# Optimization experiments

Measured on AMD Instinct MI355X. Metric: run time of the kernel, lower is better.

## Reference

```python
import jax, jax.numpy as jnp
import numpy as np

E = 8          # num_experts
D = 512        # embed_dim
FF = 4         # ff_mult
H = D * FF     # hidden
B, N = 4, 2048
TOP_K = 2


def setup_inputs() -> dict:
    key = jax.random.key(0)
    ks = jax.random.split(key, 6)
    tokens = jax.random.normal(ks[0], (B, N, D), dtype=jnp.float32)
    # token-choice top-k routing: logits -> top-2 experts per token
    logits = jax.random.normal(ks[1], (B, N, E), dtype=jnp.float32)
    topv, topi = jax.lax.top_k(logits, TOP_K)            # (B,N,K)
    disp = jnp.zeros((B, N, E), jnp.float32)
    disp = jnp.take_along_axis(disp, topi, axis=-1)  # placeholder shape trick avoided below
    disp = jnp.zeros((B, N, E), jnp.float32).at[
        jnp.arange(B)[:, None, None], jnp.arange(N)[None, :, None], topi
    ].set(1.0)                                            # (B,N,E) 0/1 dispatch mask
    w = jax.nn.softmax(topv, axis=-1)                     # combine weights over selected
    comb = jnp.zeros((B, N, E), jnp.float32).at[
        jnp.arange(B)[:, None, None], jnp.arange(N)[None, :, None], topi
    ].set(w)
    # expert params (xavier-ish scale); out_proj gain 0.02 as in module init
    Wg = jax.random.normal(ks[2], (E, D, H), dtype=jnp.float32) * (2.0 / (D + H)) ** 0.5
    Wv = jax.random.normal(ks[3], (E, D, H), dtype=jnp.float32) * (2.0 / (D + H)) ** 0.5
    Wo = jax.random.normal(ks[4], (E, H, D), dtype=jnp.float32) * 0.02 * (2.0 / (D + H)) ** 0.5
    scales = jnp.full((E,), 1.0 / E, dtype=jnp.float32)   # output_scale per expert
    return {"tokens": tokens, "dispatch_weights": disp, "combine_weights": comb,
            "Wg": Wg, "Wv": Wv, "Wo": Wo, "scales": scales}


def reference(tokens, dispatch_weights, combine_weights, Wg, Wv, Wo, scales):
    """ExpertPool.forward: per-expert SwiGLU FFN, combined by routing weights.

    Dense-masked formulation (same math as gather->FFN->weighted scatter-add:
    expert outputs only contribute where dispatch>0).
    """
    b, n, d = tokens.shape
    x = tokens.reshape(b * n, d)                          # (M, D)
    gate = jax.nn.gelu(jnp.einsum('md,edh->emh', x, Wg), approximate=False)
    value = jnp.einsum('md,edh->emh', x, Wv)
    out_e = jnp.einsum('emh,ehd->emd', gate * value, Wo) * scales[:, None, None]
    mask = dispatch_weights.reshape(b * n, -1) > 0        # (M, E)
    w = jnp.where(mask, combine_weights.reshape(b * n, -1), 0.0)
    out = jnp.einsum('emd,me->md', out_e, w)              # weighted combine
    return out.reshape(b, n, d)
```

## Files before the change

kernel.cpp:

```cpp
#include <hip/hip_runtime.h>
#include <hip/hip_bf16.h>


#define NEXP 8
#define DIM 512
#define HID 2048
#define MTOK 8192
#define PMAX (2*MTOK)
#define TM 128
#define MT 144

typedef __bf16 bf16;
typedef __bf16 bf16x8 __attribute__((ext_vector_type(8)));
typedef float  f32x4  __attribute__((ext_vector_type(4)));

#define WAITVM(N) asm volatile("s_waitcnt vmcnt(" #N ")" ::: "memory")
#define SCHED0    __builtin_amdgcn_sched_barrier(0)
#define BAR       __builtin_amdgcn_s_barrier

__device__ __forceinline__ void gload16(const bf16* g, bf16* l) {
  __builtin_amdgcn_global_load_lds(
      (const __attribute__((address_space(1))) void*)g,
      (__attribute__((address_space(3))) void*)l, 16, 0, 0);
}

__device__ __forceinline__ float gelu_f(float x){
  float s = x * 0.70710678118654752f;
  float a = fabsf(s);
  float t = 1.0f / fmaf(0.3275911f, a, 1.0f);
  float p = t*(0.254829592f + t*(-0.284496736f + t*(1.421413741f +
            t*(-1.453152027f + t*1.061405429f))));
  float er = 1.0f - p*__expf(-s*s);
  er = copysignf(er, s);
  return 0.5f*x*(1.0f + er);
}

__global__ __launch_bounds__(256) void k_prep(const float* __restrict__ tokens,
    bf16* __restrict__ Xb,
    const float* __restrict__ Wg, const float* __restrict__ Wv,
    const float* __restrict__ Wo,
    bf16* __restrict__ WgT, bf16* __restrict__ WvT, bf16* __restrict__ WoT,
    const float* __restrict__ disp, int* __restrict__ cnt) {
  __shared__ __align__(16) bf16 t[64][72];
  __shared__ int lc[NEXP];
  const int b = blockIdx.x, tid = threadIdx.x;

  if (b < 4096) {
    int i = b*256 + tid;
    float4 v = ((const float4* __restrict__)tokens)[i];
    bf16 o[4];
    o[0]=(bf16)v.x; o[1]=(bf16)v.y; o[2]=(bf16)v.z; o[3]=(bf16)v.w;
    *(uint2*)&Xb[(size_t)i*4] = *(uint2*)o;
    return;
  }
  if (b < 10240) {
    const float* pin; bf16* pout; int R, C, c0, r0;
    if (b < 8192) {
      int u = b - 4096;
      int bx = u&31, by = (u>>5)&7, z = u>>8;
      int e = z & (NEXP-1);
      pin  = ((z < NEXP) ? Wg : Wv) + (size_t)e*DIM*HID;
      pout = ((z < NEXP) ? WgT : WvT) + (size_t)e*DIM*HID;
      R = DIM; C = HID; c0 = bx*64; r0 = by*64;
    } else {
      int u = b - 8192;
      int bx = u&7, by = (u>>3)&31, z = u>>8;
      pin  = Wo  + (size_t)z*HID*DIM;
      pout = WoT + (size_t)z*HID*DIM;
      R = HID; C = DIM; c0 = bx*64; r0 = by*64;
    }
    {
      const int rr = tid>>4, cc4 = (tid&15)*4;
#pragma unroll
      for (int i=0;i<4;i++){
        int r = i*16 + rr;
        float4 v = *(const float4*)&pin[(size_t)(r0+r)*C + c0 + cc4];
        t[cc4+0][r]=(bf16)v.x; t[cc4+1][r]=(bf16)v.y;
        t[cc4+2][r]=(bf16)v.z; t[cc4+3][r]=(bf16)v.w;
      }
    }
    __syncthreads();
    {
      const int rr8 = tid>>3, cc8 = (tid&7)*8;
#pragma unroll
      for (int i=0;i<2;i++){
        int c = i*32 + rr8;
        *(uint4*)&pout[(size_t)(c0+c)*R + r0 + cc8] = *(const uint4*)&t[c][cc8];
      }
    }
    return;
  }
  {
    if (tid < NEXP) lc[tid] = 0;
    __syncthreads();
    int m = (b - 10240)*256 + tid;
    float4 d0 = *(const float4*)&disp[(size_t)m*NEXP];
    float4 d1 = *(const float4*)&disp[(size_t)m*NEXP+4];
    if (d0.x>0.f) atomicAdd(&lc[0],1);
    if (d0.y>0.f) atomicAdd(&lc[1],1);
    if (d0.z>0.f) atomicAdd(&lc[2],1);
    if (d0.w>0.f) atomicAdd(&lc[3],1);
    if (d1.x>0.f) atomicAdd(&lc[4],1);
    if (d1.y>0.f) atomicAdd(&lc[5],1);
    if (d1.z>0.f) atomicAdd(&lc[6],1);
    if (d1.w>0.f) atomicAdd(&lc[7],1);
    __syncthreads();
    if (tid < NEXP) atomicAdd(&cnt[tid], lc[tid]);
  }
}

__global__ void k_scan(const int* __restrict__ cnt, int* __restrict__ base,
                       int* __restrict__ te, int* __restrict__ trow, int* __restrict__ tn) {
  __shared__ int sb[NEXP+1], st[NEXP+1], sc[NEXP];
  if (threadIdx.x == 0){
    int b=0, t=0;
    for (int e=0;e<NEXP;e++){
      sb[e]=b; st[e]=t; sc[e]=cnt[e]; base[e]=b;
      b += sc[e];
      t += (sc[e]+TM-1)/TM;
    }
    sb[NEXP]=b; st[NEXP]=t;
  }
  __syncthreads();
  for (int idx=threadIdx.x; idx<MT; idx+=blockDim.x){
    int e=-1;
#pragma unroll
    for (int q=0;q<NEXP;q++) if (idx>=st[q] && idx<st[q+1]) e=q;
    if (e>=0){
      int k = idx - st[e];
      int nr = sc[e] - k*TM; if (nr>TM) nr=TM;
      te[idx]=e; trow[idx]=sb[e]+k*TM; tn[idx]=nr;
    } else te[idx]=-1;
  }
}

__global__ __launch_bounds__(256) void k_fill(const float* __restrict__ disp,
    const float* __restrict__ comb, const float* __restrict__ scales,
    const int* __restrict__ base, int* __restrict__ fillc,
    int* __restrict__ stok, float* __restrict__ sw, int* __restrict__ sslot) {
  int m = blockIdx.x*256 + threadIdx.x;
  int jj = 0;
#pragma unroll
  for (int e=0;e<NEXP;e++){
    float dv = disp[(size_t)m*NEXP + e];
    if (dv > 0.f) {
      int s = atomicAdd(&fillc[e], 1);
      int g = base[e] + s;
      stok[g] = m;
      sw[g] = comb[(size_t)m*NEXP + e] * scales[e];
      if (jj < 2) sslot[m*2 + jj] = g;
      jj++;
    }
  }
}

__global__ __launch_bounds__(256) void k_gemm1(const bf16* __restrict__ Xb,
    const bf16* __restrict__ WgT, const bf16* __restrict__ WvT,
    const int* __restrict__ te, const int* __restrict__ trow, const int* __restrict__ tn,
    const int* __restrict__ stok, bf16* __restrict__ H1) {
  const int tile = blockIdx.y;
  const int e = te[tile];
  if (e < 0) return;
  const int row0 = trow[tile], nrows = tn[tile];
  const int n0 = blockIdx.x*64;
  __shared__ __align__(16) bf16 Al[2*128*32];
  __shared__ __align__(16) bf16 Bgl[2*64*32];
  __shared__ __align__(16) bf16 Bvl[2*64*32];
  const int tid = threadIdx.x, lane = tid&63;
  const int wr = (tid>>7)&1, wc = (tid>>6)&1;
  const bf16* __restrict__ wg = WgT + (size_t)e*HID*DIM;
  const bf16* __restrict__ wv = WvT + (size_t)e*HID*DIM;

  const bf16* asrc[2];
#pragma unroll
  for (int i=0;i<2;i++){
    int c = i*256 + tid;
    int r = c>>2, qs = (c&3) ^ ((r>>1)&3);
    int gr = (r < nrows) ? (row0 + r) : row0;
    asrc[i] = Xb + (size_t)stok[gr]*DIM + qs*8;
  }
  const bf16 *bsg, *bsv;
  {
    int r = tid>>2, qs = (tid&3) ^ ((r>>1)&3);
    size_t o = (size_t)(n0 + r)*DIM + qs*8;
    bsg = wg + o; bsv = wv + o;
  }
  const int wbase = (tid&192)*8;

  auto stage = [&](int bi, int kt){
    const int k0 = kt*32;
    gload16(asrc[0]+k0, Al + bi*4096 + wbase);
    gload16(asrc[1]+k0, Al + bi*4096 + 2048 + wbase);
    gload16(bsg+k0, Bgl + bi*2048 + wbase);
    gload16(bsv+k0, Bvl + bi*2048 + wbase);
  };

  f32x4 accg[4][2] = {}, accv[4][2] = {};
  const int r15 = lane&15;
  const int koff = ((lane>>4) ^ ((r15>>1)&3))*8;
  stage(0, 0);
  for (int kt=0; kt<DIM/32; ++kt){
    const int bi = kt&1;
    if (kt+1 < DIM/32){ stage(bi^1, kt+1); WAITVM(4); }
    else WAITVM(0);
    BAR(); SCHED0;
    bf16x8 a[4], bg[2], bv[2];
#pragma unroll
    for (int ni=0; ni<2; ni++){
      bg[ni] = *(const bf16x8*)&Bgl[bi*2048 + (wc*32 + ni*16 + r15)*32 + koff];
      bv[ni] = *(const bf16x8*)&Bvl[bi*2048 + (wc*32 + ni*16 + r15)*32 + koff];
    }
#pragma unroll
    for (int mi=0; mi<4; mi++)
      a[mi] = *(const bf16x8*)&Al[bi*4096 + (wr*64 + mi*16 + r15)*32 + koff];
#pragma unroll
    for (int mi=0; mi<4; mi++)
#pragma unroll
      for (int ni=0; ni<2; ni++){
        accg[mi][ni] = __builtin_amdgcn_mfma_f32_16x16x32_bf16(a[mi], bg[ni], accg[mi][ni], 0,0,0);
        accv[mi][ni] = __builtin_amdgcn_mfma_f32_16x16x32_bf16(a[mi], bv[ni], accv[mi][ni], 0,0,0);
      }
    BAR(); SCHED0;
  }
  const int cb = n0 + wc*32 + r15;
  const int rb = wr*64 + (lane>>4)*4;
#pragma unroll
  for (int mi=0; mi<4; mi++)
#pragma unroll
    for (int j=0; j<4; j++){
      int r = rb + mi*16 + j;
      if (r < nrows){
#pragma unroll
        for (int ni=0; ni<2; ni++){
          float g = accg[mi][ni][j], v = accv[mi][ni][j];
          H1[(size_t)(row0+r)*HID + cb + ni*16] = (bf16)(gelu_f(g)*v);
        }
      }
    }
}

__global__ __launch_bounds__(256) void k_gemm2(const bf16* __restrict__ H1,
    const bf16* __restrict__ WoT,
    const int* __restrict__ te, const int* __restrict__ trow, const int* __restrict__ tn,
    const float* __restrict__ sw, bf16* __restrict__ gout) {
  const int L = blockIdx.x;
  const int tile = (L&7)*18 + (L>>5);
  const int n0 = ((L>>3)&3)*128;
  const int e = te[tile];
  if (e < 0) return;
  const int row0 = trow[tile], nrows = tn[tile];
  __shared__ __align__(16) bf16 Al[2*128*32];
  __shared__ __align__(16) bf16 Bl[2*128*32];
  const int tid = threadIdx.x, lane = tid&63;
  const int wr = (tid>>7)&1, wc = (tid>>6)&1;
  const bf16* __restrict__ wo = WoT + (size_t)e*DIM*HID;

  const bf16 *asrc[2], *bsrc[2];
#pragma unroll
  for (int i=0;i<2;i++){
    int c = i*256 + tid;
    int r = c>>2, qs = (c&3) ^ ((r>>1)&3);
    int ar = (r < nrows) ? (row0 + r) : row0;
    asrc[i] = H1 + (size_t)ar*HID + qs*8;
    bsrc[i] = wo + (size_t)(n0 + r)*HID + qs*8;
  }
  const int wbase = (tid&192)*8;

  auto stage = [&](int bi, int kt){
    const int k0 = kt*32;
#pragma unroll
    for (int i=0;i<2;i++){
      gload16(asrc[i]+k0, Al + bi*4096 + i*2048 + wbase);
      gload16(bsrc[i]+k0, Bl + bi*4096 + i*2048 + wbase);
    }
  };

  f32x4 acc[4][4] = {};
  const int r15 = lane&15;
  const int koff = ((lane>>4) ^ ((r15>>1)&3))*8;
  stage(0, 0);
  for (int kt=0; kt<HID/32; ++kt){
    const int bi = kt&1;
    if (kt+1 < HID/32){ stage(bi^1, kt+1); WAITVM(4); }
    else WAITVM(0);
    BAR(); SCHED0;
    bf16x8 a[4], b[4];
#pragma unroll
    for (int ni=0; ni<4; ni++)
      b[ni] = *(const bf16x8*)&Bl[bi*4096 + (wc*64 + ni*16 + r15)*32 + koff];
#pragma unroll
    for (int mi=0; mi<4; mi++)
      a[mi] = *(const bf16x8*)&Al[bi*4096 + (wr*64 + mi*16 + r15)*32 + koff];
#pragma unroll
    for (int mi=0; mi<4; mi++)
#pragma unroll
      for (int ni=0; ni<4; ni++)
        acc[mi][ni] = __builtin_amdgcn_mfma_f32_16x16x32_bf16(a[mi], b[ni], acc[mi][ni], 0,0,0);
    BAR(); SCHED0;
  }
  const int cb = n0 + wc*64 + r15;
  const int rb = wr*64 + (lane>>4)*4;
#pragma unroll
  for (int mi=0; mi<4; mi++)
#pragma unroll
    for (int j=0; j<4; j++){
      int r = rb + mi*16 + j;
      if (r < nrows){
        int slot = row0 + r;
        float wgt = sw[slot];
        bf16* op = gout + (size_t)slot*DIM + cb;
#pragma unroll
        for (int ni=0; ni<4; ni++)
          op[ni*16] = (bf16)(acc[mi][ni][j] * wgt);
      }
    }
}

__global__ __launch_bounds__(256) void k_comb(const bf16* __restrict__ gout,
    const int* __restrict__ sslot, float* __restrict__ out) {
  int idx = blockIdx.x*256 + threadIdx.x;
  int m = idx >> 7, c4 = (idx & 127)*4;
  int s0 = sslot[m*2], s1 = sslot[m*2+1];
  const bf16* p0 = gout + (size_t)s0*DIM + c4;
  const bf16* p1 = gout + (size_t)s1*DIM + c4;
  bf16 a0[4], a1[4];
  *(uint2*)a0 = *(const uint2*)p0;
  *(uint2*)a1 = *(const uint2*)p1;
  float4 x;
  x.x = (float)a0[0] + (float)a1[0];
  x.y = (float)a0[1] + (float)a1[1];
  x.z = (float)a0[2] + (float)a1[2];
  x.w = (float)a0[3] + (float)a1[3];
  *(float4*)&out[(size_t)m*DIM + c4] = x;
}

extern "C" void kernel_launch(void* const* d_in, const int* in_sizes, int n_in,
                              void* d_out, int out_size, void* d_ws, size_t ws_size,
                              hipStream_t stream) {
  const float* tokens = (const float*)d_in[0];
  const float* disp   = (const float*)d_in[1];
  const float* comb   = (const float*)d_in[2];
  const float* Wg     = (const float*)d_in[3];
  const float* Wv     = (const float*)d_in[4];
  const float* Wo     = (const float*)d_in[5];
  const float* scales = (const float*)d_in[6];
  float* out = (float*)d_out;

  size_t off = 0;
  char* wsb = (char*)d_ws;
  auto take = [&](size_t bytes)->char* {
    char* q = wsb + off; off += (bytes + 255) & ~(size_t)255; return q;
  };
  int*   cnt   = (int*)  take(NEXP*4);
  int*   basee = (int*)  take(NEXP*4);
  int*   fillc = (int*)  take(NEXP*4);
  int*   te    = (int*)  take(MT*4);
  int*   trow  = (int*)  take(MT*4);
  int*   tnr   = (int*)  take(MT*4);
  int*   stok  = (int*)  take((size_t)PMAX*4);
  float* sw    = (float*)take((size_t)PMAX*4);
  int*   sslot = (int*)  take((size_t)MTOK*2*4);
  bf16*  Xb    = (bf16*) take((size_t)MTOK*DIM*2);
  bf16*  WgT   = (bf16*) take((size_t)NEXP*DIM*HID*2);
  bf16*  WvT   = (bf16*) take((size_t)NEXP*DIM*HID*2);
  bf16*  WoT   = (bf16*) take((size_t)NEXP*DIM*HID*2);
  bf16*  H1    = (bf16*) take((size_t)PMAX*HID*2);
  bf16*  gout  = WgT;
  (void)ws_size; (void)in_sizes; (void)n_in; (void)out_size;

  hipMemsetAsync(d_ws, 0, 768, stream);

  k_prep <<<dim3(10272), 256, 0, stream>>>(tokens, Xb, Wg, Wv, Wo,
                                           WgT, WvT, WoT, disp, cnt);
  k_scan <<<1, 64, 0, stream>>>(cnt, basee, te, trow, tnr);
  k_fill <<<dim3(MTOK/256), 256, 0, stream>>>(disp, comb, scales, basee, fillc, stok, sw, sslot);
  k_gemm1<<<dim3(HID/64, MT), 256, 0, stream>>>(Xb, WgT, WvT, te, trow, tnr, stok, H1);
  k_gemm2<<<dim3(8*18*4), 256, 0, stream>>>(H1, WoT, te, trow, tnr, sw, gout);
  k_comb <<<dim3(MTOK*DIM/4/256), 256, 0, stream>>>(gout, sslot, out);
}
```

Before: 206.6 us.

## Remove scan kernel and pre-gather bf16 tokens into expert-sorted rows

Drops the separate scan kernel, so the GEMM kernels compute their tile-to-expert mapping inline from the expert counts. Token bf16 conversion moves out of the prep kernel into the fill kernel, which writes each token directly to its two permuted slots. GEMM1 then reads contiguous rows instead of indirecting through a token index array. This saves one launch and the indirect gather, but the fill kernel now does serialized per-token work in 32 threads and writes twice as many bf16 rows.

```diff
diff --git a/kernel.cpp b/kernel.cpp
--- a/kernel.cpp
+++ b/kernel.cpp
@@ -35,8 +35,25 @@
   return 0.5f*x*(1.0f + er);
 }
 
-__global__ __launch_bounds__(256) void k_prep(const float* __restrict__ tokens,
-    bf16* __restrict__ Xb,
+__device__ __forceinline__ bool tile_map(const int* __restrict__ cnt, int T,
+                                         int& row0, int& nrows) {
+  int sb = 0, stt = 0; bool ok = false;
+#pragma unroll
+  for (int q=0; q<NEXP; q++){
+    int c = cnt[q];
+    int nt = (c + TM-1)/TM;
+    if (!ok && T >= stt && T < stt+nt){
+      int k = T - stt;
+      row0 = sb + k*TM;
+      int nr = c - k*TM; if (nr > TM) nr = TM;
+      nrows = nr; ok = true;
+    }
+    stt += nt; sb += c;
+  }
+  return ok;
+}
+
+__global__ __launch_bounds__(256) void k_prep(
     const float* __restrict__ Wg, const float* __restrict__ Wv,
     const float* __restrict__ Wo,
     bf16* __restrict__ WgT, bf16* __restrict__ WvT, bf16* __restrict__ WoT,
@@ -45,25 +62,17 @@
   __shared__ int lc[NEXP];
   const int b = blockIdx.x, tid = threadIdx.x;
 
-  if (b < 4096) {
-    int i = b*256 + tid;
-    float4 v = ((const float4* __restrict__)tokens)[i];
-    bf16 o[4];
-    o[0]=(bf16)v.x; o[1]=(bf16)v.y; o[2]=(bf16)v.z; o[3]=(bf16)v.w;
-    *(uint2*)&Xb[(size_t)i*4] = *(uint2*)o;
-    return;
-  }
-  if (b < 10240) {
+  if (b < 6144) {
     const float* pin; bf16* pout; int R, C, c0, r0;
-    if (b < 8192) {
-      int u = b - 4096;
+    if (b < 4096) {
+      int u = b;
       int bx = u&31, by = (u>>5)&7, z = u>>8;
       int e = z & (NEXP-1);
       pin  = ((z < NEXP) ? Wg : Wv) + (size_t)e*DIM*HID;
       pout = ((z < NEXP) ? WgT : WvT) + (size_t)e*DIM*HID;
       R = DIM; C = HID; c0 = bx*64; r0 = by*64;
     } else {
-      int u = b - 8192;
+      int u = b - 4096;
       int bx = u&7, by = (u>>3)&31, z = u>>8;
       pin  = Wo  + (size_t)z*HID*DIM;
       pout = WoT + (size_t)z*HID*DIM;
@@ -93,7 +102,7 @@
   {
     if (tid < NEXP) lc[tid] = 0;
     __syncthreads();
-    int m = (b - 10240)*256 + tid;
+    int m = (b - 6144)*256 + tid;
     float4 d0 = *(const float4*)&disp[(size_t)m*NEXP];
     float4 d1 = *(const float4*)&disp[(size_t)m*NEXP+4];
     if (d0.x>0.f) atomicAdd(&lc[0],1);
@@ -109,65 +118,62 @@
   }
 }
 
-__global__ void k_scan(const int* __restrict__ cnt, int* __restrict__ base,
-                       int* __restrict__ te, int* __restrict__ trow, int* __restrict__ tn) {
-  __shared__ int sb[NEXP+1], st[NEXP+1], sc[NEXP];
-  if (threadIdx.x == 0){
-    int b=0, t=0;
-    for (int e=0;e<NEXP;e++){
-      sb[e]=b; st[e]=t; sc[e]=cnt[e]; base[e]=b;
-      b += sc[e];
-      t += (sc[e]+TM-1)/TM;
-    }
-    sb[NEXP]=b; st[NEXP]=t;
-  }
-  __syncthreads();
-  for (int idx=threadIdx.x; idx<MT; idx+=blockDim.x){
-    int e=-1;
-#pragma unroll
-    for (int q=0;q<NEXP;q++) if (idx>=st[q] && idx<st[q+1]) e=q;
-    if (e>=0){
-      int k = idx - st[e];
-      int nr = sc[e] - k*TM; if (nr>TM) nr=TM;
-      te[idx]=e; trow[idx]=sb[e]+k*TM; tn[idx]=nr;
-    } else te[idx]=-1;
-  }
-}
-
 __global__ __launch_bounds__(256) void k_fill(const float* __restrict__ disp,
     const float* __restrict__ comb, const float* __restrict__ scales,
-    const int* __restrict__ base, int* __restrict__ fillc,
-    int* __restrict__ stok, float* __restrict__ sw, int* __restrict__ sslot) {
-  int m = blockIdx.x*256 + threadIdx.x;
-  int jj = 0;
-#pragma unroll
-  for (int e=0;e<NEXP;e++){
-    float dv = disp[(size_t)m*NEXP + e];
-    if (dv > 0.f) {
-      int s = atomicAdd(&fillc[e], 1);
-      int g = base[e] + s;
-      stok[g] = m;
-      sw[g] = comb[(size_t)m*NEXP + e] * scales[e];
-      if (jj < 2) sslot[m*2 + jj] = g;
-      jj++;
-    }
-  }
-}
-
-__global__ __launch_bounds__(256) void k_gemm1(const bf16* __restrict__ Xb,
+    const float* __restrict__ tokens, const int* __restrict__ cnt,
+    int* __restrict__ fillc, float* __restrict__ sw, int* __restrict__ sslot,
+    bf16* __restrict__ Xg) {
+  __shared__ int sl[64];
+  const int tid = threadIdx.x;
+  if (tid < 32){
+    int m = blockIdx.x*32 + tid;
+    int base[NEXP]; int b = 0;
+#pragma unroll
+    for (int e=0;e<NEXP;e++){ base[e] = b; b += cnt[e]; }
+    int jj = 0;
+#pragma unroll
+    for (int e=0;e<NEXP;e++){
+      float dv = disp[(size_t)m*NEXP + e];
+      if (dv > 0.f) {
+        int s = atomicAdd(&fillc[e], 1);
+        int g = base[e] + s;
+        sw[g] = comb[(size_t)m*NEXP + e] * scales[e];
+        if (jj < 2){ sslot[m*2 + jj] = g; sl[tid*2 + jj] = g; }
+        jj++;
+      }
+    }
+  }
+  __syncthreads();
+  for (int t=0; t<32; t++){
+    int m = blockIdx.x*32 + t;
+    float2 v = *(const float2*)&tokens[(size_t)m*DIM + tid*2];
+    bf16 o[2]; o[0]=(bf16)v.x; o[1]=(bf16)v.y;
+    unsigned u = *(unsigned*)o;
+    int g0 = sl[t*2], g1 = sl[t*2+1];
+    *(unsigned*)&Xg[(size_t)g0*DIM + tid*2] = u;
+    *(unsigned*)&Xg[(size_t)g1*DIM + tid*2] = u;
+  }
+}
+
+__global__ __launch_bounds__(256) void k_gemm1(const bf16* __restrict__ Xg,
     const bf16* __restrict__ WgT, const bf16* __restrict__ WvT,
-    const int* __restrict__ te, const int* __restrict__ trow, const int* __restrict__ tn,
-    const int* __restrict__ stok, bf16* __restrict__ H1) {
-  const int tile = blockIdx.y;
-  const int e = te[tile];
-  if (e < 0) return;
-  const int row0 = trow[tile], nrows = tn[tile];
+    const int* __restrict__ cnt, bf16* __restrict__ H1) {
+  int row0, nrows;
+  if (!tile_map(cnt, blockIdx.y, row0, nrows)) return;
   const int n0 = blockIdx.x*64;
   __shared__ __align__(16) bf16 Al[2*128*32];
   __shared__ __align__(16) bf16 Bgl[2*64*32];
   __shared__ __align__(16) bf16 Bvl[2*64*32];
   const int tid = threadIdx.x, lane = tid&63;
   const int wr = (tid>>7)&1, wc = (tid>>6)&1;
+  int eb = 0, e = 0;
+#pragma unroll
+  for (int q=0;q<NEXP;q++){ if (row0 >= eb) e = q; eb += cnt[q]; }
+  {
+    int b2 = 0;
+#pragma unroll
+    for (int q=0;q<NEXP;q++){ if (row0 >= b2 && row0 < b2+cnt[q]) e = q; b2 += cnt[q]; }
+  }
   const bf16* __restrict__ wg = WgT + (size_t)e*HID*DIM;
   const bf16* __restrict__ wv = WvT + (size_t)e*HID*DIM;
 
@@ -177,7 +183,7 @@
     int c = i*256 + tid;
     int r = c>>2, qs = (c&3) ^ ((r>>1)&3);
     int gr = (r < nrows) ? (row0 + r) : row0;
-    asrc[i] = Xb + (size_t)stok[gr]*DIM + qs*8;
+    asrc[i] = Xg + (size_t)gr*DIM + qs*8;
   }
   const bf16 *bsg, *bsv;
   {
@@ -240,19 +246,23 @@
 }
 
 __global__ __launch_bounds__(256) void k_gemm2(const bf16* __restrict__ H1,
-    const bf16* __restrict__ WoT,
-    const int* __restrict__ te, const int* __restrict__ trow, const int* __restrict__ tn,
+    const bf16* __restrict__ WoT, const int* __restrict__ cnt,
     const float* __restrict__ sw, bf16* __restrict__ gout) {
   const int L = blockIdx.x;
-  const int tile = (L&7)*18 + (L>>5);
+  const int T = (L&7)*18 + (L>>5);
   const int n0 = ((L>>3)&3)*128;
-  const int e = te[tile];
-  if (e < 0) return;
-  const int row0 = trow[tile], nrows = tn[tile];
+  int row0, nrows;
+  if (!tile_map(cnt, T, row0, nrows)) return;
   __shared__ __align__(16) bf16 Al[2*128*32];
   __shared__ __align__(16) bf16 Bl[2*128*32];
   const int tid = threadIdx.x, lane = tid&63;
   const int wr = (tid>>7)&1, wc = (tid>>6)&1;
+  int e = 0;
+  {
+    int b2 = 0;
+#pragma unroll
+    for (int q=0;q<NEXP;q++){ if (row0 >= b2 && row0 < b2+cnt[q]) e = q; b2 += cnt[q]; }
+  }
   const bf16* __restrict__ wo = WoT + (size_t)e*DIM*HID;
 
   const bf16 *asrc[2], *bsrc[2];
@@ -352,15 +362,10 @@
     char* q = wsb + off; off += (bytes + 255) & ~(size_t)255; return q;
   };
   int*   cnt   = (int*)  take(NEXP*4);
-  int*   basee = (int*)  take(NEXP*4);
   int*   fillc = (int*)  take(NEXP*4);
-  int*   te    = (int*)  take(MT*4);
-  int*   trow  = (int*)  take(MT*4);
-  int*   tnr   = (int*)  take(MT*4);
-  int*   stok  = (int*)  take((size_t)PMAX*4);
   float* sw    = (float*)take((size_t)PMAX*4);
   int*   sslot = (int*)  take((size_t)MTOK*2*4);
-  bf16*  Xb    = (bf16*) take((size_t)MTOK*DIM*2);
+  bf16*  Xg    = (bf16*) take((size_t)PMAX*DIM*2);
   bf16*  WgT   = (bf16*) take((size_t)NEXP*DIM*HID*2);
   bf16*  WvT   = (bf16*) take((size_t)NEXP*DIM*HID*2);
   bf16*  WoT   = (bf16*) take((size_t)NEXP*DIM*HID*2);
@@ -368,13 +373,12 @@
   bf16*  gout  = WgT;
   (void)ws_size; (void)in_sizes; (void)n_in; (void)out_size;
 
-  hipMemsetAsync(d_ws, 0, 768, stream);
-
-  k_prep <<<dim3(10272), 256, 0, stream>>>(tokens, Xb, Wg, Wv, Wo,
-                                           WgT, WvT, WoT, disp, cnt);
-  k_scan <<<1, 64, 0, stream>>>(cnt, basee, te, trow, tnr);
-  k_fill <<<dim3(MTOK/256), 256, 0, stream>>>(disp, comb, scales, basee, fillc, stok, sw, sslot);
-  k_gemm1<<<dim3(HID/64, MT), 256, 0, stream>>>(Xb, WgT, WvT, te, trow, tnr, stok, H1);
-  k_gemm2<<<dim3(8*18*4), 256, 0, stream>>>(H1, WoT, te, trow, tnr, sw, gout);
+  hipMemsetAsync(d_ws, 0, 512, stream);
+
+  k_prep <<<dim3(6176), 256, 0, stream>>>(Wg, Wv, Wo, WgT, WvT, WoT, disp, cnt);
+  k_fill <<<dim3(MTOK/32), 256, 0, stream>>>(disp, comb, scales, tokens, cnt,
+                                             fillc, sw, sslot, Xg);
+  k_gemm1<<<dim3(HID/64, MT), 256, 0, stream>>>(Xg, WgT, WvT, cnt, H1);
+  k_gemm2<<<dim3(8*18*4), 256, 0, stream>>>(H1, WoT, cnt, sw, gout);
   k_comb <<<dim3(MTOK*DIM/4/256), 256, 0, stream>>>(gout, sslot, out);
 }
```

Result: slower. 219.1 us (+6.1%).
